# Kernel tuning notes

Measured on AMD Instinct MI355X. Metric: run time of the kernel, lower is better.

The kernel has to match this reference:

```python
import jax, jax.numpy as jnp
import numpy as np

N = 100000
E = 600000
H = 128
L = 2  # mp_ngcn


def setup_inputs() -> dict:
    key = jax.random.key(0)
    k = jax.random.split(key, 8)
    h = jax.random.normal(k[0], (N, H), dtype=jnp.float32)
    edge_row = jax.random.randint(k[1], (E,), 0, N, dtype=jnp.int32)
    edge_col = jax.random.randint(k[2], (E,), 0, N, dtype=jnp.int32)
    edge_w = jax.random.uniform(k[3], (E,), dtype=jnp.float32)
    # xavier_normal gain=1.414 for square fc: std = 1.414*sqrt(2/(H+H))
    std = 1.414 * np.sqrt(2.0 / (H + H))
    fc_w = jax.random.normal(k[4], (L, H, H), dtype=jnp.float32) * std
    fc_b = jnp.zeros((L, H), dtype=jnp.float32)           # init 0.0
    gcn_bias = jnp.full((L, H), 0.001, dtype=jnp.float32)  # init 0.001
    prelu_a = jnp.full((L,), 0.25, dtype=jnp.float32)      # PReLU default
    return {"h": h, "edge_row": edge_row, "edge_col": edge_col,
            "edge_w": edge_w, "fc_w": fc_w, "fc_b": fc_b,
            "gcn_bias": gcn_bias, "prelu_a": prelu_a}


def reference(h, edge_row, edge_col, edge_w, fc_w, fc_b, gcn_bias, prelu_a):
    x = h
    for i in range(L):
        # dense linear transform: [N,H] @ [H,H]^T + b
        s = x @ fc_w[i].T + fc_b[i]
        # sparse adjacency spmm: out[r] = sum_e w_e * s[c_e]
        msg = s[edge_col] * edge_w[:, None]        # [E,H] gather + scale
        out = jax.ops.segment_sum(msg, edge_row, num_segments=N)
        out = out + gcn_bias[i]
        # dropout (eval-mode identity), then PReLU
        x = jnp.where(out > 0, out, prelu_a[i] * out)
    return x
```

## Files before the change

kernel.cpp:

```cpp
#include <hip/hip_runtime.h>

#define H 128

typedef __attribute__((ext_vector_type(8))) short bf16x8;
typedef __attribute__((ext_vector_type(4))) short s16x4;
typedef __attribute__((ext_vector_type(4))) float f32x4;

__device__ inline unsigned short f2bf(float f) {
    unsigned u = __float_as_uint(f);
    unsigned r = (u + 0x7fffu + ((u >> 16) & 1u)) >> 16;
    return (unsigned short)r;
}
__device__ inline float bflo(unsigned u) { return __uint_as_float(u << 16); }
__device__ inline float bfhi(unsigned u) { return __uint_as_float(u & 0xffff0000u); }

__device__ inline unsigned pack_cw(int c, float w) {
    unsigned q = (unsigned)(w * 32768.f);
    if (q > 32767u) q = 32767u;
    return ((unsigned)c << 15) | q;
}

#define MB 64

template<bool BF16IN>
__device__ __forceinline__ void gemm_body(
    short* wlds, const void* __restrict__ xv, const float* __restrict__ W,
    const float* __restrict__ b, short* __restrict__ s_out, int N, int nbatch,
    int bid, int grid)
{
    const int t = threadIdx.x;
    const int l = t & 63;
    const int w = t >> 6;
    const int n_g   = (w & 1) * 32;
    const int col_g = (w >> 1) * 64;
    const int ln15 = l & 15;
    const int lhi  = l >> 4;

    #pragma unroll
    for (int i = 0; i < 16; ++i) {
        int fidx = i * 256 + t;
        int j  = fidx >> 5;
        int c4 = fidx & 31;
        float4 v = *reinterpret_cast<const float4*>(W + (size_t)j * H + c4 * 4);
        s16x4 p;
        p[0] = (short)f2bf(v.x); p[1] = (short)f2bf(v.y);
        p[2] = (short)f2bf(v.z); p[3] = (short)f2bf(v.w);
        *reinterpret_cast<s16x4*>(&wlds[j * 136 + c4 * 4]) = p;
    }

    float4 bias4[4];
    #pragma unroll
    for (int jt = 0; jt < 4; ++jt)
        bias4[jt] = *reinterpret_cast<const float4*>(b + col_g + jt * 16 + lhi * 4);

    __syncthreads();

    for (int batch = bid; batch < nbatch; batch += grid) {
        const int row0 = batch * MB;

        bf16x8 ax[4][2];
        #pragma unroll
        for (int nf = 0; nf < 2; ++nf) {
            const int n = row0 + n_g + nf * 16 + ln15;
            const bool ok = (n < N);
            #pragma unroll
            for (int ks = 0; ks < 4; ++ks) {
                bf16x8 f = {0, 0, 0, 0, 0, 0, 0, 0};
                if (ok) {
                    if (BF16IN) {
                        f = *reinterpret_cast<const bf16x8*>(
                            (const short*)xv + (size_t)n * H + ks * 32 + lhi * 8);
                    } else {
                        const float* p = (const float*)xv + (size_t)n * H + ks * 32 + lhi * 8;
                        float4 lo = *reinterpret_cast<const float4*>(p);
                        float4 hi = *reinterpret_cast<const float4*>(p + 4);
                        f[0] = (short)f2bf(lo.x); f[1] = (short)f2bf(lo.y);
                        f[2] = (short)f2bf(lo.z); f[3] = (short)f2bf(lo.w);
                        f[4] = (short)f2bf(hi.x); f[5] = (short)f2bf(hi.y);
                        f[6] = (short)f2bf(hi.z); f[7] = (short)f2bf(hi.w);
                    }
                }
                ax[ks][nf] = f;
            }
        }

        f32x4 acc[2][4] = {};
        #pragma unroll
        for (int ks = 0; ks < 4; ++ks) {
            #pragma unroll
            for (int jt = 0; jt < 4; ++jt) {
                bf16x8 aw = *reinterpret_cast<const bf16x8*>(
                    &wlds[(col_g + jt * 16 + ln15) * 136 + ks * 32 + lhi * 8]);
                acc[0][jt] = __builtin_amdgcn_mfma_f32_16x16x32_bf16(
                    aw, ax[ks][0], acc[0][jt], 0, 0, 0);
                acc[1][jt] = __builtin_amdgcn_mfma_f32_16x16x32_bf16(
                    aw, ax[ks][1], acc[1][jt], 0, 0, 0);
            }
        }

        #pragma unroll
        for (int nf = 0; nf < 2; ++nf) {
            const int n = row0 + n_g + nf * 16 + ln15;
            if (n < N) {
                #pragma unroll
                for (int jt = 0; jt < 4; ++jt) {
                    s16x4 p;
                    p[0] = (short)f2bf(acc[nf][jt][0] + bias4[jt].x);
                    p[1] = (short)f2bf(acc[nf][jt][1] + bias4[jt].y);
                    p[2] = (short)f2bf(acc[nf][jt][2] + bias4[jt].z);
                    p[3] = (short)f2bf(acc[nf][jt][3] + bias4[jt].w);
                    *reinterpret_cast<s16x4*>(
                        s_out + (size_t)n * H + col_g + jt * 16 + lhi * 4) = p;
                }
            }
        }
    }
}

template<bool BF16IN>
__global__ __launch_bounds__(256) void gemm_mfma_kernel(
    const void* __restrict__ xv, const float* __restrict__ W,
    const float* __restrict__ b, short* __restrict__ s_out, int N, int nbatch)
{
    __shared__ short wlds[H * 136];
    gemm_body<BF16IN>(wlds, xv, W, b, s_out, N, nbatch, blockIdx.x, gridDim.x);
}

__global__ __launch_bounds__(256) void count_plus_gemm_kernel(
    const int* __restrict__ erow, int* __restrict__ counts,
    int* __restrict__ rank, int E, int count_blocks,
    const void* __restrict__ xv, const float* __restrict__ W,
    const float* __restrict__ b, short* __restrict__ s_out, int N, int nbatch,
    int gemm_grid)
{
    __shared__ short wlds[H * 136];
    if ((int)blockIdx.x < count_blocks) {
        int e = blockIdx.x * 256 + threadIdx.x;
        if (e < E) rank[e] = atomicAdd(&counts[erow[e]], 1);
        return;
    }
    gemm_body<false>(wlds, xv, W, b, s_out, N, nbatch,
                     (int)blockIdx.x - count_blocks, gemm_grid);
}

__global__ __launch_bounds__(256) void zero_kernel(int4* __restrict__ p, int n4)
{
    int i = blockIdx.x * blockDim.x + threadIdx.x;
    if (i < n4) p[i] = make_int4(0, 0, 0, 0);
}

#define SCAN_BLK 1024
__global__ __launch_bounds__(SCAN_BLK) void scan_block_kernel(
    const int* __restrict__ counts, int* __restrict__ incl,
    int* __restrict__ bsums, int N)
{
    __shared__ int sm[SCAN_BLK];
    int i = blockIdx.x * SCAN_BLK + threadIdx.x;
    int v = (i < N) ? counts[i] : 0;
    sm[threadIdx.x] = v;
    __syncthreads();
    for (int off = 1; off < SCAN_BLK; off <<= 1) {
        int tv = (threadIdx.x >= off) ? sm[threadIdx.x - off] : 0;
        __syncthreads();
        sm[threadIdx.x] += tv;
        __syncthreads();
    }
    if (i < N) incl[i] = sm[threadIdx.x];
    if (threadIdx.x == SCAN_BLK - 1) bsums[blockIdx.x] = sm[SCAN_BLK - 1];
}

__global__ __launch_bounds__(SCAN_BLK) void finalize_offsets_kernel(
    const int* __restrict__ counts, const int* __restrict__ incl,
    const int* __restrict__ bsums, int* __restrict__ offsets, int N, int E, int nb)
{
    __shared__ int sb[SCAN_BLK];
    int tid = threadIdx.x;
    sb[tid] = (tid < nb) ? bsums[tid] : 0;
    __syncthreads();
    int prefix = 0;
    const int bid = blockIdx.x;
    for (int j = 0; j < bid; ++j) prefix += sb[j];

    int i = bid * SCAN_BLK + tid;
    if (i < N) offsets[i] = incl[i] - counts[i] + prefix;
    if (i == 0) offsets[N] = E;
}

__global__ __launch_bounds__(256) void fill_kernel(
    const int* __restrict__ erow, const int* __restrict__ ecol,
    const float* __restrict__ ew, const int* __restrict__ offsets,
    const int* __restrict__ rank, unsigned* __restrict__ cw, int E)
{
    int e = blockIdx.x * blockDim.x + threadIdx.x;
    if (e < E) {
        int r = erow[e];
        cw[offsets[r] + rank[e]] = pack_cw(ecol[e], ew[e]);
    }
}

template<int MODE>
__global__ __launch_bounds__(256) void spmm_csr2_kernel(
    const int* __restrict__ offsets, const unsigned* __restrict__ cw,
    const short* __restrict__ s_bf, const float* __restrict__ gbias,
    const float* __restrict__ a_ptr, float* __restrict__ out_f,
    short* __restrict__ out_b, int N)
{
    const float a = a_ptr[0];
    int gid = blockIdx.x * blockDim.x + threadIdx.x;
    int wid  = gid >> 6;
    int l    = gid & 63;
    int half = l >> 5;
    int li   = l & 31;
    int r = wid * 2 + half;
    if (r >= N) return;

    const int beg = offsets[r], end = offsets[r + 1];
    const size_t coff = (size_t)li * 4;
    const float SC = 1.f / 32768.f;

    float a00=0.f,a01=0.f,a02=0.f,a03=0.f;
    float a10=0.f,a11=0.f,a12=0.f,a13=0.f;
    float a20=0.f,a21=0.f,a22=0.f,a23=0.f;
    float a30=0.f,a31=0.f,a32=0.f,a33=0.f;

    int e = beg;
    for (; e + 4 <= end; e += 4) {
        unsigned p0 = cw[e],     p1 = cw[e + 1];
        unsigned p2 = cw[e + 2], p3 = cw[e + 3];
        float w0 = (float)(p0 & 0x7fffu) * SC;
        float w1 = (float)(p1 & 0x7fffu) * SC;
        float w2 = (float)(p2 & 0x7fffu) * SC;
        float w3 = (float)(p3 & 0x7fffu) * SC;
        unsigned long long u0 = *reinterpret_cast<const unsigned long long*>(
            s_bf + (size_t)(p0 >> 15) * H + coff);
        unsigned long long u1 = *reinterpret_cast<const unsigned long long*>(
            s_bf + (size_t)(p1 >> 15) * H + coff);
        unsigned long long u2 = *reinterpret_cast<const unsigned long long*>(
            s_bf + (size_t)(p2 >> 15) * H + coff);
        unsigned long long u3 = *reinterpret_cast<const unsigned long long*>(
            s_bf + (size_t)(p3 >> 15) * H + coff);
        unsigned lo;
        lo = (unsigned)u0; a00 += w0 * bflo(lo); a01 += w0 * bfhi(lo);
        lo = (unsigned)(u0 >> 32); a02 += w0 * bflo(lo); a03 += w0 * bfhi(lo);
        lo = (unsigned)u1; a10 += w1 * bflo(lo); a11 += w1 * bfhi(lo);
        lo = (unsigned)(u1 >> 32); a12 += w1 * bflo(lo); a13 += w1 * bfhi(lo);
        lo = (unsigned)u2; a20 += w2 * bflo(lo); a21 += w2 * bfhi(lo);
        lo = (unsigned)(u2 >> 32); a22 += w2 * bflo(lo); a23 += w2 * bfhi(lo);
        lo = (unsigned)u3; a30 += w3 * bflo(lo); a31 += w3 * bfhi(lo);
        lo = (unsigned)(u3 >> 32); a32 += w3 * bflo(lo); a33 += w3 * bfhi(lo);
    }
    for (; e < end; ++e) {
        unsigned p0 = cw[e];
        float w0 = (float)(p0 & 0x7fffu) * SC;
        unsigned long long u0 = *reinterpret_cast<const unsigned long long*>(
            s_bf + (size_t)(p0 >> 15) * H + coff);
        unsigned lo;
        lo = (unsigned)u0; a00 += w0 * bflo(lo); a01 += w0 * bfhi(lo);
        lo = (unsigned)(u0 >> 32); a02 += w0 * bflo(lo); a03 += w0 * bfhi(lo);
    }

    float4 g = *reinterpret_cast<const float4*>(gbias + li * 4);
    float v0 = (a00 + a10) + (a20 + a30) + g.x;
    float v1 = (a01 + a11) + (a21 + a31) + g.y;
    float v2 = (a02 + a12) + (a22 + a32) + g.z;
    float v3 = (a03 + a13) + (a23 + a33) + g.w;
    v0 = v0 > 0.f ? v0 : a * v0;
    v1 = v1 > 0.f ? v1 : a * v1;
    v2 = v2 > 0.f ? v2 : a * v2;
    v3 = v3 > 0.f ? v3 : a * v3;

    if (MODE == 0) {
        *reinterpret_cast<float4*>(out_f + (size_t)r * H + li * 4) =
            make_float4(v0, v1, v2, v3);
    } else {
        s16x4 p;
        p[0] = (short)f2bf(v0); p[1] = (short)f2bf(v1);
        p[2] = (short)f2bf(v2); p[3] = (short)f2bf(v3);
        *reinterpret_cast<s16x4*>(out_b + (size_t)r * H + li * 4) = p;
    }
}

__global__ __launch_bounds__(256) void init_out_kernel(
    float* __restrict__ out, const float* __restrict__ gbias, int total4)
{
    int i = blockIdx.x * blockDim.x + threadIdx.x;
    const int stride = gridDim.x * blockDim.x;
    for (; i < total4; i += stride) {
        int c4 = i & 31;
        float4 bv = *reinterpret_cast<const float4*>(gbias + c4 * 4);
        *reinterpret_cast<float4*>(out + (size_t)i * 4) = bv;
    }
}

__global__ __launch_bounds__(256) void spmm_edge_kernel(
    const int* __restrict__ erow, const int* __restrict__ ecol,
    const float* __restrict__ ew, const short* __restrict__ s_bf,
    float* __restrict__ out, int E)
{
    long long gid = (long long)blockIdx.x * blockDim.x + threadIdx.x;
    int e = (int)(gid >> 6);
    int l = (int)(gid & 63);
    if (e >= E) return;
    int r = erow[e];
    int c = ecol[e];
    float w = ew[e];
    unsigned u = *reinterpret_cast<const unsigned*>(s_bf + (size_t)c * H + 2 * l);
    unsafeAtomicAdd(out + (size_t)r * H + l * 2 + 0, bflo(u) * w);
    unsafeAtomicAdd(out + (size_t)r * H + l * 2 + 1, bfhi(u) * w);
}

__global__ __launch_bounds__(256) void prelu_kernel(
    float* __restrict__ buf, const float* __restrict__ a_ptr, int total4)
{
    const float a = a_ptr[0];
    int i = blockIdx.x * blockDim.x + threadIdx.x;
    const int stride = gridDim.x * blockDim.x;
    for (; i < total4; i += stride) {
        float4 v = *reinterpret_cast<float4*>(buf + (size_t)i * 4);
        v.x = v.x > 0.f ? v.x : a * v.x;
        v.y = v.y > 0.f ? v.y : a * v.y;
        v.z = v.z > 0.f ? v.z : a * v.z;
        v.w = v.w > 0.f ? v.w : a * v.w;
        *reinterpret_cast<float4*>(buf + (size_t)i * 4) = v;
    }
}

extern "C" void kernel_launch(void* const* d_in, const int* in_sizes, int n_in,
                              void* d_out, int out_size, void* d_ws, size_t ws_size,
                              hipStream_t stream)
{
    const float* h        = (const float*)d_in[0];
    const int*   erow     = (const int*)d_in[1];
    const int*   ecol     = (const int*)d_in[2];
    const float* ew       = (const float*)d_in[3];
    const float* fc_w     = (const float*)d_in[4];
    const float* fc_b     = (const float*)d_in[5];
    const float* gcn_bias = (const float*)d_in[6];
    const float* prelu_a  = (const float*)d_in[7];

    const int N = in_sizes[0] / H;
    const int E = in_sizes[1];
    float* out = (float*)d_out;

    char* ws = (char*)d_ws;
    short* s_bf  = (short*)ws;
    size_t off = (size_t)N * H * sizeof(short);
    short* x1_bf = (short*)(ws + off); off += (size_t)N * H * sizeof(short);
    off = (off + 15) & ~(size_t)15;
    int* counts  = (int*)(ws + off); off += (size_t)((N + 3) & ~3) * 4;
    int* incl    = (int*)(ws + off); off += (size_t)N * 4;
    int* offsets = (int*)(ws + off); off += (size_t)(N + 1) * 4;
    const int nb_scan = (N + SCAN_BLK - 1) / SCAN_BLK;
    int* bsums   = (int*)(ws + off); off += (size_t)nb_scan * 4;
    int* rank    = (int*)(ws + off); off += (size_t)E * 4;
    unsigned* cw = (unsigned*)(ws + off); off += (size_t)E * 4;

    const int eblocks = (E + 255) / 256;
    const int nbatch = (N + MB - 1) / MB;
    const int ggrid = nbatch < 1024 ? nbatch : 1024;

    if (off <= ws_size) {
        const int n4 = (N + 3) / 4;
        zero_kernel<<<(n4 + 255) / 256, 256, 0, stream>>>((int4*)counts, n4);
        count_plus_gemm_kernel<<<eblocks + ggrid, 256, 0, stream>>>(
            erow, counts, rank, E, eblocks,
            h, fc_w, fc_b, s_bf, N, nbatch, ggrid);
        scan_block_kernel<<<nb_scan, SCAN_BLK, 0, stream>>>(counts, incl, bsums, N);
        finalize_offsets_kernel<<<nb_scan, SCAN_BLK, 0, stream>>>(
            counts, incl, bsums, offsets, N, E, nb_scan);
        fill_kernel<<<eblocks, 256, 0, stream>>>(erow, ecol, ew, offsets, rank, cw, E);

        const int spmm_blocks = (int)((((long long)(N + 1) / 2) * 64 + 255) / 256);

        spmm_csr2_kernel<1><<<spmm_blocks, 256, 0, stream>>>(
            offsets, cw, s_bf, gcn_bias, prelu_a, nullptr, x1_bf, N);
        gemm_mfma_kernel<true><<<ggrid, 256, 0, stream>>>(
            x1_bf, fc_w + H * H, fc_b + H, s_bf, N, nbatch);
        spmm_csr2_kernel<0><<<spmm_blocks, 256, 0, stream>>>(
            offsets, cw, s_bf, gcn_bias + H, prelu_a + 1, out, nullptr, N);
    } else {
        const int total4 = N * (H / 4);
        const int spmm_blocks = (int)(((long long)E * 64 + 255) / 256);

        gemm_mfma_kernel<false><<<ggrid, 256, 0, stream>>>(h, fc_w, fc_b, s_bf, N, nbatch);
        init_out_kernel<<<2048, 256, 0, stream>>>(out, gcn_bias, total4);
        spmm_edge_kernel<<<spmm_blocks, 256, 0, stream>>>(erow, ecol, ew, s_bf, out, E);
        prelu_kernel<<<2048, 256, 0, stream>>>(out, prelu_a, total4);

        gemm_mfma_kernel<false><<<ggrid, 256, 0, stream>>>(out, fc_w + H * H, fc_b + H, s_bf, N, nbatch);
        init_out_kernel<<<2048, 256, 0, stream>>>(out, gcn_bias + H, total4);
        spmm_edge_kernel<<<spmm_blocks, 256, 0, stream>>>(erow, ecol, ew, s_bf, out, E);
        prelu_kernel<<<2048, 256, 0, stream>>>(out, prelu_a + 1, total4);
    }
}
```

Baseline: 157.8 us.

## Use 16 lanes per row in SpMM and split count from GEMM kernel

The CSR SpMM now assigns 16 lanes per destination row instead of 32. Each lane gathers 16 bytes (8 bf16 values) per edge, so a wavefront processes four rows at once with wider loads and fewer accumulator registers. The fused count+GEMM kernel is split back into a separate atomic count kernel and a standalone GEMM launch. That removes the co-scheduling of the two but adds one launch. Wider per-lane loads may improve memory-level parallelism, though per-row load balancing changes.

```diff
diff --git a/kernel.cpp b/kernel.cpp
--- a/kernel.cpp
+++ b/kernel.cpp
@@ -23,11 +23,12 @@
 #define MB 64
 
 template<bool BF16IN>
-__device__ __forceinline__ void gemm_body(
-    short* wlds, const void* __restrict__ xv, const float* __restrict__ W,
-    const float* __restrict__ b, short* __restrict__ s_out, int N, int nbatch,
-    int bid, int grid)
-{
+__global__ __launch_bounds__(256) void gemm_mfma_kernel(
+    const void* __restrict__ xv, const float* __restrict__ W,
+    const float* __restrict__ b, short* __restrict__ s_out, int N, int nbatch)
+{
+    __shared__ short wlds[H * 136];
+
     const int t = threadIdx.x;
     const int l = t & 63;
     const int w = t >> 6;
@@ -55,7 +56,7 @@
 
     __syncthreads();
 
-    for (int batch = bid; batch < nbatch; batch += grid) {
+    for (int batch = blockIdx.x; batch < nbatch; batch += gridDim.x) {
         const int row0 = batch * MB;
 
         bf16x8 ax[4][2];
@@ -117,36 +118,18 @@
     }
 }
 
-template<bool BF16IN>
-__global__ __launch_bounds__(256) void gemm_mfma_kernel(
-    const void* __restrict__ xv, const float* __restrict__ W,
-    const float* __restrict__ b, short* __restrict__ s_out, int N, int nbatch)
-{
-    __shared__ short wlds[H * 136];
-    gemm_body<BF16IN>(wlds, xv, W, b, s_out, N, nbatch, blockIdx.x, gridDim.x);
-}
-
-__global__ __launch_bounds__(256) void count_plus_gemm_kernel(
-    const int* __restrict__ erow, int* __restrict__ counts,
-    int* __restrict__ rank, int E, int count_blocks,
-    const void* __restrict__ xv, const float* __restrict__ W,
-    const float* __restrict__ b, short* __restrict__ s_out, int N, int nbatch,
-    int gemm_grid)
-{
-    __shared__ short wlds[H * 136];
-    if ((int)blockIdx.x < count_blocks) {
-        int e = blockIdx.x * 256 + threadIdx.x;
-        if (e < E) rank[e] = atomicAdd(&counts[erow[e]], 1);
-        return;
-    }
-    gemm_body<false>(wlds, xv, W, b, s_out, N, nbatch,
-                     (int)blockIdx.x - count_blocks, gemm_grid);
-}
-
 __global__ __launch_bounds__(256) void zero_kernel(int4* __restrict__ p, int n4)
 {
     int i = blockIdx.x * blockDim.x + threadIdx.x;
     if (i < n4) p[i] = make_int4(0, 0, 0, 0);
+}
+
+__global__ __launch_bounds__(256) void count_rank_kernel(
+    const int* __restrict__ erow, int* __restrict__ counts,
+    int* __restrict__ rank, int E)
+{
+    int e = blockIdx.x * blockDim.x + threadIdx.x;
+    if (e < E) rank[e] = atomicAdd(&counts[erow[e]], 1);
 }
 
 #define SCAN_BLK 1024
@@ -199,7 +182,7 @@
 }
 
 template<int MODE>
-__global__ __launch_bounds__(256) void spmm_csr2_kernel(
+__global__ __launch_bounds__(256) void spmm_csr3_kernel(
     const int* __restrict__ offsets, const unsigned* __restrict__ cw,
     const short* __restrict__ s_bf, const float* __restrict__ gbias,
     const float* __restrict__ a_ptr, float* __restrict__ out_f,
@@ -207,21 +190,18 @@
 {
     const float a = a_ptr[0];
     int gid = blockIdx.x * blockDim.x + threadIdx.x;
-    int wid  = gid >> 6;
-    int l    = gid & 63;
-    int half = l >> 5;
-    int li   = l & 31;
-    int r = wid * 2 + half;
+    int wid = gid >> 6;
+    int l   = gid & 63;
+    int sub = l >> 4;
+    int li  = l & 15;
+    int r = wid * 4 + sub;
     if (r >= N) return;
 
     const int beg = offsets[r], end = offsets[r + 1];
-    const size_t coff = (size_t)li * 4;
+    const size_t coff = (size_t)li * 8;
     const float SC = 1.f / 32768.f;
 
-    float a00=0.f,a01=0.f,a02=0.f,a03=0.f;
-    float a10=0.f,a11=0.f,a12=0.f,a13=0.f;
-    float a20=0.f,a21=0.f,a22=0.f,a23=0.f;
-    float a30=0.f,a31=0.f,a32=0.f,a33=0.f;
+    float a0=0.f,a1=0.f,a2=0.f,a3=0.f,a4=0.f,a5=0.f,a6=0.f,a7=0.f;
 
     int e = beg;
     for (; e + 4 <= end; e += 4) {
@@ -231,52 +211,58 @@
         float w1 = (float)(p1 & 0x7fffu) * SC;
         float w2 = (float)(p2 & 0x7fffu) * SC;
         float w3 = (float)(p3 & 0x7fffu) * SC;
-        unsigned long long u0 = *reinterpret_cast<const unsigned long long*>(
-            s_bf + (size_t)(p0 >> 15) * H + coff);
-        unsigned long long u1 = *reinterpret_cast<const unsigned long long*>(
-            s_bf + (size_t)(p1 >> 15) * H + coff);
-        unsigned long long u2 = *reinterpret_cast<const unsigned long long*>(
-            s_bf + (size_t)(p2 >> 15) * H + coff);
-        unsigned long long u3 = *reinterpret_cast<const unsigned long long*>(
-            s_bf + (size_t)(p3 >> 15) * H + coff);
-        unsigned lo;
-        lo = (unsigned)u0; a00 += w0 * bflo(lo); a01 += w0 * bfhi(lo);
-        lo = (unsigned)(u0 >> 32); a02 += w0 * bflo(lo); a03 += w0 * bfhi(lo);
-        lo = (unsigned)u1; a10 += w1 * bflo(lo); a11 += w1 * bfhi(lo);
-        lo = (unsigned)(u1 >> 32); a12 += w1 * bflo(lo); a13 += w1 * bfhi(lo);
-        lo = (unsigned)u2; a20 += w2 * bflo(lo); a21 += w2 * bfhi(lo);
-        lo = (unsigned)(u2 >> 32); a22 += w2 * bflo(lo); a23 += w2 * bfhi(lo);
-        lo = (unsigned)u3; a30 += w3 * bflo(lo); a31 += w3 * bfhi(lo);
-        lo = (unsigned)(u3 >> 32); a32 += w3 * bflo(lo); a33 += w3 * bfhi(lo);
+        uint4 u0 = *reinterpret_cast<const uint4*>(s_bf + (size_t)(p0 >> 15) * H + coff);
+        uint4 u1 = *reinterpret_cast<const uint4*>(s_bf + (size_t)(p1 >> 15) * H + coff);
+        uint4 u2 = *reinterpret_cast<const uint4*>(s_bf + (size_t)(p2 >> 15) * H + coff);
+        uint4 u3 = *reinterpret_cast<const uint4*>(s_bf + (size_t)(p3 >> 15) * H + coff);
+        a0 += w0 * bflo(u0.x); a1 += w0 * bfhi(u0.x);
+        a2 += w0 * bflo(u0.y); a3 += w0 * bfhi(u0.y);
+        a4 += w0 * bflo(u0.z); a5 += w0 * bfhi(u0.z);
+        a6 += w0 * bflo(u0.w); a7 += w0 * bfhi(u0.w);
+        a0 += w1 * bflo(u1.x); a1 += w1 * bfhi(u1.x);
+        a2 += w1 * bflo(u1.y); a3 += w1 * bfhi(u1.y);
+        a4 += w1 * bflo(u1.z); a5 += w1 * bfhi(u1.z);
+        a6 += w1 * bflo(u1.w); a7 += w1 * bfhi(u1.w);
+        a0 += w2 * bflo(u2.x); a1 += w2 * bfhi(u2.x);
+        a2 += w2 * bflo(u2.y); a3 += w2 * bfhi(u2.y);
+        a4 += w2 * bflo(u2.z); a5 += w2 * bfhi(u2.z);
+        a6 += w2 * bflo(u2.w); a7 += w2 * bfhi(u2.w);
+        a0 += w3 * bflo(u3.x); a1 += w3 * bfhi(u3.x);
+        a2 += w3 * bflo(u3.y); a3 += w3 * bfhi(u3.y);
+        a4 += w3 * bflo(u3.z); a5 += w3 * bfhi(u3.z);
+        a6 += w3 * bflo(u3.w); a7 += w3 * bfhi(u3.w);
     }
     for (; e < end; ++e) {
         unsigned p0 = cw[e];
         float w0 = (float)(p0 & 0x7fffu) * SC;
-        unsigned long long u0 = *reinterpret_cast<const unsigned long long*>(
-            s_bf + (size_t)(p0 >> 15) * H + coff);
-        unsigned lo;
-        lo = (unsigned)u0; a00 += w0 * bflo(lo); a01 += w0 * bfhi(lo);
-        lo = (unsigned)(u0 >> 32); a02 += w0 * bflo(lo); a03 += w0 * bfhi(lo);
-    }
-
-    float4 g = *reinterpret_cast<const float4*>(gbias + li * 4);
-    float v0 = (a00 + a10) + (a20 + a30) + g.x;
-    float v1 = (a01 + a11) + (a21 + a31) + g.y;
-    float v2 = (a02 + a12) + (a22 + a32) + g.z;
-    float v3 = (a03 + a13) + (a23 + a33) + g.w;
-    v0 = v0 > 0.f ? v0 : a * v0;
-    v1 = v1 > 0.f ? v1 : a * v1;
-    v2 = v2 > 0.f ? v2 : a * v2;
-    v3 = v3 > 0.f ? v3 : a * v3;
+        uint4 u0 = *reinterpret_cast<const uint4*>(s_bf + (size_t)(p0 >> 15) * H + coff);
+        a0 += w0 * bflo(u0.x); a1 += w0 * bfhi(u0.x);
+        a2 += w0 * bflo(u0.y); a3 += w0 * bfhi(u0.y);
+        a4 += w0 * bflo(u0.z); a5 += w0 * bfhi(u0.z);
+        a6 += w0 * bflo(u0.w); a7 += w0 * bfhi(u0.w);
+    }
+
+    float4 g0 = *reinterpret_cast<const float4*>(gbias + li * 8);
+    float4 g1 = *reinterpret_cast<const float4*>(gbias + li * 8 + 4);
+    float v0 = a0 + g0.x, v1 = a1 + g0.y, v2 = a2 + g0.z, v3 = a3 + g0.w;
+    float v4 = a4 + g1.x, v5 = a5 + g1.y, v6 = a6 + g1.z, v7 = a7 + g1.w;
+    v0 = v0 > 0.f ? v0 : a * v0;  v1 = v1 > 0.f ? v1 : a * v1;
+    v2 = v2 > 0.f ? v2 : a * v2;  v3 = v3 > 0.f ? v3 : a * v3;
+    v4 = v4 > 0.f ? v4 : a * v4;  v5 = v5 > 0.f ? v5 : a * v5;
+    v6 = v6 > 0.f ? v6 : a * v6;  v7 = v7 > 0.f ? v7 : a * v7;
 
     if (MODE == 0) {
-        *reinterpret_cast<float4*>(out_f + (size_t)r * H + li * 4) =
+        *reinterpret_cast<float4*>(out_f + (size_t)r * H + li * 8) =
             make_float4(v0, v1, v2, v3);
+        *reinterpret_cast<float4*>(out_f + (size_t)r * H + li * 8 + 4) =
+            make_float4(v4, v5, v6, v7);
     } else {
-        s16x4 p;
+        bf16x8 p;
         p[0] = (short)f2bf(v0); p[1] = (short)f2bf(v1);
         p[2] = (short)f2bf(v2); p[3] = (short)f2bf(v3);
-        *reinterpret_cast<s16x4*>(out_b + (size_t)r * H + li * 4) = p;
+        p[4] = (short)f2bf(v4); p[5] = (short)f2bf(v5);
+        p[6] = (short)f2bf(v6); p[7] = (short)f2bf(v7);
+        *reinterpret_cast<bf16x8*>(out_b + (size_t)r * H + li * 8) = p;
     }
 }
 
@@ -362,21 +348,20 @@
     if (off <= ws_size) {
         const int n4 = (N + 3) / 4;
         zero_kernel<<<(n4 + 255) / 256, 256, 0, stream>>>((int4*)counts, n4);
-        count_plus_gemm_kernel<<<eblocks + ggrid, 256, 0, stream>>>(
-            erow, counts, rank, E, eblocks,
-            h, fc_w, fc_b, s_bf, N, nbatch, ggrid);
+        count_rank_kernel<<<eblocks, 256, 0, stream>>>(erow, counts, rank, E);
         scan_block_kernel<<<nb_scan, SCAN_BLK, 0, stream>>>(counts, incl, bsums, N);
         finalize_offsets_kernel<<<nb_scan, SCAN_BLK, 0, stream>>>(
             counts, incl, bsums, offsets, N, E, nb_scan);
         fill_kernel<<<eblocks, 256, 0, stream>>>(erow, ecol, ew, offsets, rank, cw, E);
 
-        const int spmm_blocks = (int)((((long long)(N + 1) / 2) * 64 + 255) / 256);
-
-        spmm_csr2_kernel<1><<<spmm_blocks, 256, 0, stream>>>(
+        const int spmm_blocks = (int)(((long long)N * 16 + 255) / 256);
+
+        gemm_mfma_kernel<false><<<ggrid, 256, 0, stream>>>(h, fc_w, fc_b, s_bf, N, nbatch);
+        spmm_csr3_kernel<1><<<spmm_blocks, 256, 0, stream>>>(
             offsets, cw, s_bf, gcn_bias, prelu_a, nullptr, x1_bf, N);
         gemm_mfma_kernel<true><<<ggrid, 256, 0, stream>>>(
             x1_bf, fc_w + H * H, fc_b + H, s_bf, N, nbatch);
-        spmm_csr2_kernel<0><<<spmm_blocks, 256, 0, stream>>>(
+        spmm_csr3_kernel<0><<<spmm_blocks, 256, 0, stream>>>(
             offsets, cw, s_bf, gcn_bias + H, prelu_a + 1, out, nullptr, N);
     } else {
         const int total4 = N * (H / 4);
```

After: 156.2 us. About the same (-1.0%).

## Fuse layer-1 SpMM+PReLU with layer-2 GEMM via LDS tile, unfuse count from GEMM

Applied to the files above, without the earlier changes.

Adds a kernel that computes the first sparse aggregation, bias and PReLU for a 64-row tile, keeps the result in LDS, and immediately runs the second-layer MFMA GEMM on it. This removes the bf16 x1 intermediate write and reread, plus one kernel launch. The edge-count atomic pass is split back out of the first GEMM into its own kernel. As a result the first GEMM no longer overlaps with counting, and the fused kernel's gather phase uses fewer, LDS-heavy blocks (768 grid, extra 17KB LDS), which may reduce latency hiding for the irregular gathers.

```diff
diff --git a/kernel.cpp b/kernel.cpp
--- a/kernel.cpp
+++ b/kernel.cpp
@@ -23,11 +23,12 @@
 #define MB 64
 
 template<bool BF16IN>
-__device__ __forceinline__ void gemm_body(
-    short* wlds, const void* __restrict__ xv, const float* __restrict__ W,
-    const float* __restrict__ b, short* __restrict__ s_out, int N, int nbatch,
-    int bid, int grid)
-{
+__global__ __launch_bounds__(256) void gemm_mfma_kernel(
+    const void* __restrict__ xv, const float* __restrict__ W,
+    const float* __restrict__ b, short* __restrict__ s_out, int N, int nbatch)
+{
+    __shared__ short wlds[H * 136];
+
     const int t = threadIdx.x;
     const int l = t & 63;
     const int w = t >> 6;
@@ -55,7 +56,7 @@
 
     __syncthreads();
 
-    for (int batch = bid; batch < nbatch; batch += grid) {
+    for (int batch = blockIdx.x; batch < nbatch; batch += gridDim.x) {
         const int row0 = batch * MB;
 
         bf16x8 ax[4][2];
@@ -117,36 +118,168 @@
     }
 }
 
-template<bool BF16IN>
-__global__ __launch_bounds__(256) void gemm_mfma_kernel(
-    const void* __restrict__ xv, const float* __restrict__ W,
-    const float* __restrict__ b, short* __restrict__ s_out, int N, int nbatch)
+__global__ __launch_bounds__(256) void fused_spmm_gemm_kernel(
+    const int* __restrict__ offsets, const unsigned* __restrict__ cw,
+    const short* __restrict__ s_bf, const float* __restrict__ gbias0,
+    const float* __restrict__ a0_ptr, const float* __restrict__ W1,
+    const float* __restrict__ b1, short* __restrict__ s2, int N, int nbatch)
 {
     __shared__ short wlds[H * 136];
-    gemm_body<BF16IN>(wlds, xv, W, b, s_out, N, nbatch, blockIdx.x, gridDim.x);
-}
-
-__global__ __launch_bounds__(256) void count_plus_gemm_kernel(
-    const int* __restrict__ erow, int* __restrict__ counts,
-    int* __restrict__ rank, int E, int count_blocks,
-    const void* __restrict__ xv, const float* __restrict__ W,
-    const float* __restrict__ b, short* __restrict__ s_out, int N, int nbatch,
-    int gemm_grid)
-{
-    __shared__ short wlds[H * 136];
-    if ((int)blockIdx.x < count_blocks) {
-        int e = blockIdx.x * 256 + threadIdx.x;
-        if (e < E) rank[e] = atomicAdd(&counts[erow[e]], 1);
-        return;
-    }
-    gemm_body<false>(wlds, xv, W, b, s_out, N, nbatch,
-                     (int)blockIdx.x - count_blocks, gemm_grid);
+    __shared__ short xlds[MB * 136];
+
+    const int t = threadIdx.x;
+    const int l = t & 63;
+    const int w = t >> 6;
+    const int half = l >> 5;
+    const int li   = l & 31;
+    const int n_g   = (w & 1) * 32;
+    const int col_g = (w >> 1) * 64;
+    const int ln15 = l & 15;
+    const int lhi  = l >> 4;
+    const float a0 = a0_ptr[0];
+    const float SC = 1.f / 32768.f;
+
+    #pragma unroll
+    for (int i = 0; i < 16; ++i) {
+        int fidx = i * 256 + t;
+        int j  = fidx >> 5;
+        int c4 = fidx & 31;
+        float4 v = *reinterpret_cast<const float4*>(W1 + (size_t)j * H + c4 * 4);
+        s16x4 p;
+        p[0] = (short)f2bf(v.x); p[1] = (short)f2bf(v.y);
+        p[2] = (short)f2bf(v.z); p[3] = (short)f2bf(v.w);
+        *reinterpret_cast<s16x4*>(&wlds[j * 136 + c4 * 4]) = p;
+    }
+
+    float4 bias4[4];
+    #pragma unroll
+    for (int jt = 0; jt < 4; ++jt)
+        bias4[jt] = *reinterpret_cast<const float4*>(b1 + col_g + jt * 16 + lhi * 4);
+
+    const float4 g0 = *reinterpret_cast<const float4*>(gbias0 + li * 4);
+
+    for (int batch = blockIdx.x; batch < nbatch; batch += gridDim.x) {
+        const int row0 = batch * MB;
+
+        __syncthreads();
+
+        for (int it = 0; it < 8; ++it) {
+            const int rl = w * 16 + it * 2 + half;
+            const int r  = row0 + rl;
+            s16x4 p = {0, 0, 0, 0};
+            if (r < N) {
+                const int beg = offsets[r], end = offsets[r + 1];
+                const size_t coff = (size_t)li * 4;
+                float a00=0.f,a01=0.f,a02=0.f,a03=0.f;
+                float a10=0.f,a11=0.f,a12=0.f,a13=0.f;
+                float a20=0.f,a21=0.f,a22=0.f,a23=0.f;
+                float a30=0.f,a31=0.f,a32=0.f,a33=0.f;
+                int e = beg;
+                for (; e + 4 <= end; e += 4) {
+                    unsigned p0 = cw[e],     p1 = cw[e + 1];
+                    unsigned p2 = cw[e + 2], p3 = cw[e + 3];
+                    float w0 = (float)(p0 & 0x7fffu) * SC;
+                    float w1v = (float)(p1 & 0x7fffu) * SC;
+                    float w2 = (float)(p2 & 0x7fffu) * SC;
+                    float w3 = (float)(p3 & 0x7fffu) * SC;
+                    unsigned long long u0 = *reinterpret_cast<const unsigned long long*>(
+                        s_bf + (size_t)(p0 >> 15) * H + coff);
+                    unsigned long long u1 = *reinterpret_cast<const unsigned long long*>(
+                        s_bf + (size_t)(p1 >> 15) * H + coff);
+                    unsigned long long u2 = *reinterpret_cast<const unsigned long long*>(
+                        s_bf + (size_t)(p2 >> 15) * H + coff);
+                    unsigned long long u3 = *reinterpret_cast<const unsigned long long*>(
+                        s_bf + (size_t)(p3 >> 15) * H + coff);
+                    unsigned lo;
+                    lo = (unsigned)u0; a00 += w0 * bflo(lo); a01 += w0 * bfhi(lo);
+                    lo = (unsigned)(u0 >> 32); a02 += w0 * bflo(lo); a03 += w0 * bfhi(lo);
+                    lo = (unsigned)u1; a10 += w1v * bflo(lo); a11 += w1v * bfhi(lo);
+                    lo = (unsigned)(u1 >> 32); a12 += w1v * bflo(lo); a13 += w1v * bfhi(lo);
+                    lo = (unsigned)u2; a20 += w2 * bflo(lo); a21 += w2 * bfhi(lo);
+                    lo = (unsigned)(u2 >> 32); a22 += w2 * bflo(lo); a23 += w2 * bfhi(lo);
+                    lo = (unsigned)u3; a30 += w3 * bflo(lo); a31 += w3 * bfhi(lo);
+                    lo = (unsigned)(u3 >> 32); a32 += w3 * bflo(lo); a33 += w3 * bfhi(lo);
+                }
+                for (; e < end; ++e) {
+                    unsigned p0 = cw[e];
+                    float w0 = (float)(p0 & 0x7fffu) * SC;
+                    unsigned long long u0 = *reinterpret_cast<const unsigned long long*>(
+                        s_bf + (size_t)(p0 >> 15) * H + coff);
+                    unsigned lo;
+                    lo = (unsigned)u0; a00 += w0 * bflo(lo); a01 += w0 * bfhi(lo);
+                    lo = (unsigned)(u0 >> 32); a02 += w0 * bflo(lo); a03 += w0 * bfhi(lo);
+                }
+                float v0 = (a00 + a10) + (a20 + a30) + g0.x;
+                float v1 = (a01 + a11) + (a21 + a31) + g0.y;
+                float v2 = (a02 + a12) + (a22 + a32) + g0.z;
+                float v3 = (a03 + a13) + (a23 + a33) + g0.w;
+                v0 = v0 > 0.f ? v0 : a0 * v0;
+                v1 = v1 > 0.f ? v1 : a0 * v1;
+                v2 = v2 > 0.f ? v2 : a0 * v2;
+                v3 = v3 > 0.f ? v3 : a0 * v3;
+                p[0] = (short)f2bf(v0); p[1] = (short)f2bf(v1);
+                p[2] = (short)f2bf(v2); p[3] = (short)f2bf(v3);
+            }
+            *reinterpret_cast<s16x4*>(&xlds[rl * 136 + li * 4]) = p;
+        }
+
+        __syncthreads();
+
+        bf16x8 ax[4][2];
+        #pragma unroll
+        for (int nf = 0; nf < 2; ++nf) {
+            const int rl = n_g + nf * 16 + ln15;
+            #pragma unroll
+            for (int ks = 0; ks < 4; ++ks)
+                ax[ks][nf] = *reinterpret_cast<const bf16x8*>(
+                    &xlds[rl * 136 + ks * 32 + lhi * 8]);
+        }
+
+        f32x4 acc[2][4] = {};
+        #pragma unroll
+        for (int ks = 0; ks < 4; ++ks) {
+            #pragma unroll
+            for (int jt = 0; jt < 4; ++jt) {
+                bf16x8 aw = *reinterpret_cast<const bf16x8*>(
+                    &wlds[(col_g + jt * 16 + ln15) * 136 + ks * 32 + lhi * 8]);
+                acc[0][jt] = __builtin_amdgcn_mfma_f32_16x16x32_bf16(
+                    aw, ax[ks][0], acc[0][jt], 0, 0, 0);
+                acc[1][jt] = __builtin_amdgcn_mfma_f32_16x16x32_bf16(
+                    aw, ax[ks][1], acc[1][jt], 0, 0, 0);
+            }
+        }
+
+        #pragma unroll
+        for (int nf = 0; nf < 2; ++nf) {
+            const int n = row0 + n_g + nf * 16 + ln15;
+            if (n < N) {
+                #pragma unroll
+                for (int jt = 0; jt < 4; ++jt) {
+                    s16x4 p;
+                    p[0] = (short)f2bf(acc[nf][jt][0] + bias4[jt].x);
+                    p[1] = (short)f2bf(acc[nf][jt][1] + bias4[jt].y);
+                    p[2] = (short)f2bf(acc[nf][jt][2] + bias4[jt].z);
+                    p[3] = (short)f2bf(acc[nf][jt][3] + bias4[jt].w);
+                    *reinterpret_cast<s16x4*>(
+                        s2 + (size_t)n * H + col_g + jt * 16 + lhi * 4) = p;
+                }
+            }
+        }
+    }
 }
 
 __global__ __launch_bounds__(256) void zero_kernel(int4* __restrict__ p, int n4)
 {
     int i = blockIdx.x * blockDim.x + threadIdx.x;
     if (i < n4) p[i] = make_int4(0, 0, 0, 0);
+}
+
+__global__ __launch_bounds__(256) void count_rank_kernel(
+    const int* __restrict__ erow, int* __restrict__ counts,
+    int* __restrict__ rank, int E)
+{
+    int e = blockIdx.x * blockDim.x + threadIdx.x;
+    if (e < E) rank[e] = atomicAdd(&counts[erow[e]], 1);
 }
 
 #define SCAN_BLK 1024
@@ -343,9 +476,9 @@
     float* out = (float*)d_out;
 
     char* ws = (char*)d_ws;
-    short* s_bf  = (short*)ws;
+    short* s_bf = (short*)ws;
     size_t off = (size_t)N * H * sizeof(short);
-    short* x1_bf = (short*)(ws + off); off += (size_t)N * H * sizeof(short);
+    short* s2   = (short*)(ws + off); off += (size_t)N * H * sizeof(short);
     off = (off + 15) & ~(size_t)15;
     int* counts  = (int*)(ws + off); off += (size_t)((N + 3) & ~3) * 4;
     int* incl    = (int*)(ws + off); off += (size_t)N * 4;
@@ -358,13 +491,12 @@
     const int eblocks = (E + 255) / 256;
     const int nbatch = (N + MB - 1) / MB;
     const int ggrid = nbatch < 1024 ? nbatch : 1024;
+    const int fgrid = nbatch < 768 ? nbatch : 768;
 
     if (off <= ws_size) {
         const int n4 = (N + 3) / 4;
         zero_kernel<<<(n4 + 255) / 256, 256, 0, stream>>>((int4*)counts, n4);
-        count_plus_gemm_kernel<<<eblocks + ggrid, 256, 0, stream>>>(
-            erow, counts, rank, E, eblocks,
-            h, fc_w, fc_b, s_bf, N, nbatch, ggrid);
+        count_rank_kernel<<<eblocks, 256, 0, stream>>>(erow, counts, rank, E);
         scan_block_kernel<<<nb_scan, SCAN_BLK, 0, stream>>>(counts, incl, bsums, N);
         finalize_offsets_kernel<<<nb_scan, SCAN_BLK, 0, stream>>>(
             counts, incl, bsums, offsets, N, E, nb_scan);
@@ -372,12 +504,12 @@
 
         const int spmm_blocks = (int)((((long long)(N + 1) / 2) * 64 + 255) / 256);
 
-        spmm_csr2_kernel<1><<<spmm_blocks, 256, 0, stream>>>(
-            offsets, cw, s_bf, gcn_bias, prelu_a, nullptr, x1_bf, N);
-        gemm_mfma_kernel<true><<<ggrid, 256, 0, stream>>>(
-            x1_bf, fc_w + H * H, fc_b + H, s_bf, N, nbatch);
+        gemm_mfma_kernel<false><<<ggrid, 256, 0, stream>>>(h, fc_w, fc_b, s_bf, N, nbatch);
+        fused_spmm_gemm_kernel<<<fgrid, 256, 0, stream>>>(
+            offsets, cw, s_bf, gcn_bias, prelu_a,
+            fc_w + H * H, fc_b + H, s2, N, nbatch);
         spmm_csr2_kernel<0><<<spmm_blocks, 256, 0, stream>>>(
-            offsets, cw, s_bf, gcn_bias + H, prelu_a + 1, out, nullptr, N);
+            offsets, cw, s2, gcn_bias + H, prelu_a + 1, out, nullptr, N);
     } else {
         const int total4 = N * (H / 4);
         const int spmm_blocks = (int)(((long long)E * 64 + 255) / 256);
```

Result: slower. 190.2 us (+20.5%).
